# Kernel tuning notes

Measured on AMD Instinct MI355X. Metric: run time of the kernel, lower is better.

Reference implementation:

```python
import jax, jax.numpy as jnp
import numpy as np
from jax import lax

B, QL, N_IN, H = 64, 2048, 256, 64


def setup_inputs() -> dict:
    key = jax.random.key(0)
    ks = jax.random.split(key, 8)
    s = 1.0 / np.sqrt(H)  # PyTorch LSTMCell init scale
    return {
        "h_concat": jax.random.normal(ks[0], (B, QL, N_IN), dtype=jnp.float32),
        "w21": jax.random.normal(ks[1], (N_IN, 1), dtype=jnp.float32),
        "w22": jax.random.normal(ks[2], (H, 1), dtype=jnp.float32),
        "bias2": jax.random.normal(ks[3], (1,), dtype=jnp.float32),
        "W_ih": jax.random.uniform(ks[4], (4 * H, N_IN + 1), dtype=jnp.float32, minval=-s, maxval=s),
        "W_hh": jax.random.uniform(ks[5], (4 * H, H), dtype=jnp.float32, minval=-s, maxval=s),
        "b_ih": jax.random.uniform(ks[6], (4 * H,), dtype=jnp.float32, minval=-s, maxval=s),
        "b_hh": jax.random.uniform(ks[7], (4 * H,), dtype=jnp.float32, minval=-s, maxval=s),
    }


def reference(h_concat, w21, w22, bias2, W_ih, W_hh, b_ih, b_hh):
    Bsz, T, n_in = h_concat.shape
    nh = W_hh.shape[1]

    def step(carry, x):
        h, c = carry  # [B,H] each; x: [B,n_in]
        # sigmoid gate: pz_t = sigmoid(x @ w21 + h @ w22 + bias2) -> [B,1]
        pz = jax.nn.sigmoid(x @ w21 + h @ w22 + bias2)
        hz = jnp.concatenate([x, pz], axis=1)  # [B, n_in+1]
        # LSTMCell (PyTorch gate order: i, f, g, o)
        gates = hz @ W_ih.T + b_ih + h @ W_hh.T + b_hh  # [B,4H]
        i, f, g, o = jnp.split(gates, 4, axis=1)
        c_new = jax.nn.sigmoid(f) * c + jax.nn.sigmoid(i) * jnp.tanh(g)
        h_new = jax.nn.sigmoid(o) * jnp.tanh(c_new)
        return (h_new, c_new), pz[:, 0]

    h0 = jnp.zeros((Bsz, nh), dtype=h_concat.dtype)
    c0 = jnp.zeros((Bsz, nh), dtype=h_concat.dtype)
    xs = jnp.swapaxes(h_concat, 0, 1)  # [T,B,n_in]
    _, Z = lax.scan(step, (h0, c0), xs)  # Z: [T,B]
    return jnp.swapaxes(Z, 0, 1)  # [B,T]
```

## Files before the change

kernel.cpp:

```cpp
#include <hip/hip_runtime.h>

#define TT 2048
#define BB 64

typedef float v2f __attribute__((ext_vector_type(2)));

__device__ __forceinline__ float frcp(float x) { return __builtin_amdgcn_rcpf(x); }
__device__ __forceinline__ float fsig(float x) { return frcp(1.f + __expf(-x)); }
__device__ __forceinline__ float ftan(float x) { return 1.f - 2.f * frcp(1.f + __expf(2.f * x)); }
__device__ __forceinline__ v2f fma2(v2f a, v2f b, v2f c) { return __builtin_elementwise_fma(a, b, c); }

__device__ __forceinline__ void barrier_lgkm() {
  asm volatile("s_waitcnt lgkmcnt(0)\n\ts_barrier" ::: "memory");
}

#define DPPADD(x, ctrl)                                                        \
  (x) += __builtin_bit_cast(float, __builtin_amdgcn_update_dpp(                \
             0, __builtin_bit_cast(int, (x)), (ctrl), 0xf, 0xf, true))

__device__ __forceinline__ float wave_sum64(float x) {
  DPPADD(x, 0x111);
  DPPADD(x, 0x112);
  DPPADD(x, 0x114);
  DPPADD(x, 0x118);
  DPPADD(x, 0x142);
  DPPADD(x, 0x143);
  return __builtin_bit_cast(
      float, __builtin_amdgcn_readlane(__builtin_bit_cast(int, x), 63));
}

__global__ __launch_bounds__(256) void gates_gemm(const float* __restrict__ X,
                                                  const float* __restrict__ W,
                                                  const float* __restrict__ bih,
                                                  const float* __restrict__ bhh,
                                                  float* __restrict__ G,
                                                  int t0, int Tc) {
  __shared__ __align__(16) float As[32][64];
  __shared__ __align__(16) float Bs[32][64];
  const int tid = threadIdx.x;
  const int m0 = blockIdx.x * 64;
  const int n0 = blockIdx.y * 64;
  const int bb = m0 / Tc;
  const int tt0 = m0 - bb * Tc;
  const int tx = tid & 15, ty = tid >> 4;
  const int r  = tid >> 2;
  const int kq = (tid & 3) * 8;
  const float* xrow = X + ((size_t)(bb * TT + t0 + tt0 + r)) * 256 + kq;
  const float* wrow = W + (size_t)(n0 + r) * 257 + kq;
  float acc[4][4] = {};
  for (int k0 = 0; k0 < 256; k0 += 32) {
    float4 a0 = *reinterpret_cast<const float4*>(xrow + k0);
    float4 a1 = *reinterpret_cast<const float4*>(xrow + k0 + 4);
    float bv[8];
#pragma unroll
    for (int u = 0; u < 8; ++u) bv[u] = wrow[k0 + u];
    if (k0 != 0) __syncthreads();
    As[kq+0][r]=a0.x; As[kq+1][r]=a0.y; As[kq+2][r]=a0.z; As[kq+3][r]=a0.w;
    As[kq+4][r]=a1.x; As[kq+5][r]=a1.y; As[kq+6][r]=a1.z; As[kq+7][r]=a1.w;
#pragma unroll
    for (int u = 0; u < 8; ++u) Bs[kq+u][r] = bv[u];
    __syncthreads();
#pragma unroll
    for (int kk = 0; kk < 32; ++kk) {
      float4 av = *reinterpret_cast<const float4*>(&As[kk][ty*4]);
      float4 bw = *reinterpret_cast<const float4*>(&Bs[kk][tx*4]);
      const float aa[4] = {av.x, av.y, av.z, av.w};
      const float bbv[4] = {bw.x, bw.y, bw.z, bw.w};
#pragma unroll
      for (int i = 0; i < 4; ++i)
#pragma unroll
        for (int j = 0; j < 4; ++j) acc[i][j] += aa[i] * bbv[j];
    }
  }
  const int col = n0 + tx * 4;
  float bsum[4];
#pragma unroll
  for (int j = 0; j < 4; ++j) bsum[j] = bih[col + j] + bhh[col + j];
#pragma unroll
  for (int i = 0; i < 4; ++i) {
    float4 o;
    o.x = acc[i][0] + bsum[0];
    o.y = acc[i][1] + bsum[1];
    o.z = acc[i][2] + bsum[2];
    o.w = acc[i][3] + bsum[3];
    *reinterpret_cast<float4*>(&G[(size_t)(m0 + ty*4 + i) * 256 + col]) = o;
  }
}

__global__ __launch_bounds__(256) void pz_kernel(const float* __restrict__ X,
                                                 const float* __restrict__ w21,
                                                 const float* __restrict__ bias2,
                                                 float* __restrict__ P,
                                                 int t0, int Tc) {
  const int r = blockIdx.x * 4 + (threadIdx.x >> 6);
  const int lane = threadIdx.x & 63;
  const int bb = r / Tc;
  const int tt = r - bb * Tc;
  const float4 xv = *reinterpret_cast<const float4*>(
      &X[((size_t)(bb * TT + t0 + tt)) * 256 + lane * 4]);
  const float4 wv = *reinterpret_cast<const float4*>(&w21[lane * 4]);
  float s = xv.x*wv.x + xv.y*wv.y + xv.z*wv.z + xv.w*wv.w;
#pragma unroll
  for (int o = 32; o; o >>= 1) s += __shfl_xor(s, o);
  if (lane == 0) P[r] = s + bias2[0];
}

__global__ __launch_bounds__(128, 1) void lstm_seq3(const float* __restrict__ G,
                                                    const float* __restrict__ P,
                                                    const float* __restrict__ Wih,
                                                    const float* __restrict__ Whh,
                                                    const float* __restrict__ w22,
                                                    float* __restrict__ Z,
                                                    float* __restrict__ hq,
                                                    float* __restrict__ cq,
                                                    int t0, int Tc) {
  const int b = blockIdx.x;
  const int tid = threadIdx.x;
  const int w = tid >> 6;
  const int l = tid & 63;
  const int sub = l >> 5;
  const int u = w * 32 + (l & 31);
  __shared__ __align__(16) float h_s[2][64];

  const int rowA = sub * 64 + u;
  const int rowB = rowA + 128;
  v2f whA[32], whB[32];
#pragma unroll
  for (int j = 0; j < 16; ++j) {
    float4 va = *reinterpret_cast<const float4*>(&Whh[(size_t)rowA * 64 + 4*j]);
    float4 vb = *reinterpret_cast<const float4*>(&Whh[(size_t)rowB * 64 + 4*j]);
    whA[2*j] = v2f{va.x, va.y}; whA[2*j+1] = v2f{va.z, va.w};
    whB[2*j] = v2f{vb.x, vb.y}; whB[2*j+1] = v2f{vb.z, vb.w};
  }
  const float wihLA = Wih[(size_t)rowA * 257 + 256];
  const float wihLB = Wih[(size_t)rowB * 257 + 256];
  const float w22r  = w22[l];
  const float kB = sub ? 1.f : 2.f;
  const float mB = sub ? 1.f : 2.f;
  const float aB = sub ? 0.f : -1.f;

  float h = 0.f, c = 0.f;
  if (t0 != 0) { h = hq[b * 64 + u]; c = cq[b * 64 + u]; }
  if (l >= 32) h_s[0][u] = h;
  barrier_lgkm();

  const float* Gb = G + (size_t)b * Tc * 256;
  const float* Pb = P + (size_t)b * Tc;
  float* Zb = Z + (size_t)b * TT + t0;

  float grA[4], grB[4], pr[4];
#pragma unroll
  for (int q = 0; q < 4; ++q) {
    grA[q] = Gb[(size_t)q * 256 + rowA];
    grB[q] = Gb[(size_t)q * 256 + rowB];
    pr[q]  = Pb[q];
  }

  for (int tt = 0; tt < Tc; tt += 4) {
    float zs[4];
#pragma unroll
    for (int uu = 0; uu < 4; ++uu) {
      const int step = tt + uu;
      const int rb = uu & 1;
      const float gxA = grA[uu], gxB = grB[uu], p0 = pr[uu];
      int pf = step + 4; if (pf > Tc - 1) pf = Tc - 1;
      grA[uu] = Gb[(size_t)pf * 256 + rowA];
      grB[uu] = Gb[(size_t)pf * 256 + rowB];
      pr[uu]  = Pb[pf];

      float rsum = h_s[rb][l] * w22r;
      const float tot = wave_sum64(rsum);
      const float pz = fsig(tot + p0);

      v2f aA0{0.f,0.f}, aA1{0.f,0.f}, aA2{0.f,0.f}, aA3{0.f,0.f};
      v2f aB0{0.f,0.f}, aB1{0.f,0.f}, aB2{0.f,0.f}, aB3{0.f,0.f};
      const float4* hp = reinterpret_cast<const float4*>(h_s[rb]);
#pragma unroll
      for (int q = 0; q < 16; q += 2) {
        const float4 hv0 = hp[q];
        const float4 hv1 = hp[q+1];
        const v2f h01 = v2f{hv0.x, hv0.y}, h23 = v2f{hv0.z, hv0.w};
        const v2f h45 = v2f{hv1.x, hv1.y}, h67 = v2f{hv1.z, hv1.w};
        aA0 = fma2(h01, whA[2*q],   aA0);  aA1 = fma2(h23, whA[2*q+1], aA1);
        aA2 = fma2(h45, whA[2*q+2], aA2);  aA3 = fma2(h67, whA[2*q+3], aA3);
        aB0 = fma2(h01, whB[2*q],   aB0);  aB1 = fma2(h23, whB[2*q+1], aB1);
        aB2 = fma2(h45, whB[2*q+2], aB2);  aB3 = fma2(h67, whB[2*q+3], aB3);
      }
      const v2f sA = (aA0 + aA1) + (aA2 + aA3);
      const v2f sB = (aB0 + aB1) + (aB2 + aB3);
      const float preA = gxA + pz * wihLA + (sA.x + sA.y);
      const float preB = gxB + pz * wihLB + (sB.x + sB.y);
      const float actA = fsig(preA);
      const float actB = mB * fsig(kB * preB) + aB;

      const float prod = actA * actB;
      const float igx = __shfl_xor(prod, 32);
      c = actA * c + igx;
      h = actB * ftan(c);
      if (l >= 32) h_s[rb ^ 1][u] = h;
      zs[uu] = pz;
      barrier_lgkm();
    }
    if (tid == 0) {
      float4 zo; zo.x = zs[0]; zo.y = zs[1]; zo.z = zs[2]; zo.w = zs[3];
      *reinterpret_cast<float4*>(&Zb[tt]) = zo;
    }
  }
  if (l >= 32) { hq[b * 64 + u] = h; cq[b * 64 + u] = c; }
}

__global__ __launch_bounds__(256) void lstm_fallback(const float* __restrict__ X,
    const float* __restrict__ w21, const float* __restrict__ w22,
    const float* __restrict__ bias2, const float* __restrict__ Wih,
    const float* __restrict__ Whh, const float* __restrict__ bih,
    const float* __restrict__ bhh, float* __restrict__ Z) {
  const int b = blockIdx.x;
  const int g = threadIdx.x;
  const int lane = g & 63;
  __shared__ __align__(16) float h_s[64];
  __shared__ float act_s[256];
  __shared__ __align__(16) float x_s[256];
  __shared__ __align__(16) float w21_s[256];
  float wh[64];
#pragma unroll
  for (int j = 0; j < 64; j += 4) {
    float4 v = *reinterpret_cast<const float4*>(&Whh[(size_t)g*64 + j]);
    wh[j]=v.x; wh[j+1]=v.y; wh[j+2]=v.z; wh[j+3]=v.w;
  }
  const float wihL = Wih[(size_t)g*257 + 256];
  const float bias = bih[g] + bhh[g];
  const float b2 = bias2[0];
  const float w22r = w22[lane];
  w21_s[g] = w21[g];
  if (g < 64) h_s[g] = 0.f;
  float c = 0.f;
  __syncthreads();
  const float* Wr = Wih + (size_t)g * 257;
  for (int t = 0; t < TT; ++t) {
    x_s[g] = X[((size_t)b*TT + t)*256 + g];
    __syncthreads();
    float pv = h_s[lane] * w22r;
    {
      const float4 xq = *reinterpret_cast<const float4*>(&x_s[lane*4]);
      const float4 wq = *reinterpret_cast<const float4*>(&w21_s[lane*4]);
      pv += xq.x*wq.x + xq.y*wq.y + xq.z*wq.z + xq.w*wq.w;
    }
#pragma unroll
    for (int o = 32; o; o >>= 1) pv += __shfl_xor(pv, o);
    const float pz = fsig(pv + b2);
    float a0=0.f, a1=0.f, a2=0.f, a3=0.f;
#pragma unroll
    for (int j = 0; j < 64; j += 4) {
      float4 hv = *reinterpret_cast<const float4*>(&h_s[j]);
      a0 += hv.x*wh[j]; a1 += hv.y*wh[j+1]; a2 += hv.z*wh[j+2]; a3 += hv.w*wh[j+3];
    }
    float xd0=0.f, xd1=0.f, xd2=0.f, xd3=0.f;
    for (int k = 0; k < 256; k += 4) {
      const float4 xq = *reinterpret_cast<const float4*>(&x_s[k]);
      xd0 += xq.x*Wr[k]; xd1 += xq.y*Wr[k+1]; xd2 += xq.z*Wr[k+2]; xd3 += xq.w*Wr[k+3];
    }
    const float pre = bias + pz*wihL + ((a0+a1)+(a2+a3)) + ((xd0+xd1)+(xd2+xd3));
    act_s[g] = ((g >> 6) == 2) ? ftan(pre) : fsig(pre);
    if (g == 0) Z[(size_t)b*TT + t] = pz;
    __syncthreads();
    if (g < 64) {
      const float iv = act_s[g], fv = act_s[64+g], gv = act_s[128+g], ov = act_s[192+g];
      c = fv*c + iv*gv;
      h_s[g] = ov * ftan(c);
    }
    __syncthreads();
  }
}

extern "C" void kernel_launch(void* const* d_in, const int* in_sizes, int n_in,
                              void* d_out, int out_size, void* d_ws, size_t ws_size,
                              hipStream_t stream) {
  const float* X     = (const float*)d_in[0];
  const float* w21   = (const float*)d_in[1];
  const float* w22   = (const float*)d_in[2];
  const float* bias2 = (const float*)d_in[3];
  const float* Wih   = (const float*)d_in[4];
  const float* Whh   = (const float*)d_in[5];
  const float* bih   = (const float*)d_in[6];
  const float* bhh   = (const float*)d_in[7];
  float* Z = (float*)d_out;

  int Tc = 0;
  for (int cand = 2048; cand >= 64; cand >>= 1) {
    size_t need = (size_t)cand * (64*256*4 + 64*4) + 2*64*64*4;
    if (ws_size >= need) { Tc = cand; break; }
  }
  if (Tc == 0) {
    lstm_fallback<<<dim3(64), dim3(256), 0, stream>>>(X, w21, w22, bias2, Wih, Whh, bih, bhh, Z);
    return;
  }
  float* Gbuf = (float*)d_ws;
  float* Pbuf = Gbuf + (size_t)64 * Tc * 256;
  float* hq   = Pbuf + (size_t)64 * Tc;
  float* cq   = hq + 64 * 64;
  for (int t0 = 0; t0 < 2048; t0 += Tc) {
    gates_gemm<<<dim3(Tc, 4), dim3(256), 0, stream>>>(X, Wih, bih, bhh, Gbuf, t0, Tc);
    pz_kernel<<<dim3(16 * Tc), dim3(256), 0, stream>>>(X, w21, bias2, Pbuf, t0, Tc);
    lstm_seq3<<<dim3(64), dim3(128), 0, stream>>>(Gbuf, Pbuf, Wih, Whh, w22, Z, hq, cq, t0, Tc);
  }
}
```

Measured before the change: 1.229 ms.

## Fuse pz projection into gates GEMM and pack four batch rows per LSTM block

```diff
diff --git a/kernel.cpp b/kernel.cpp
--- a/kernel.cpp
+++ b/kernel.cpp
@@ -2,6 +2,7 @@
 
 #define TT 2048
 #define BB 64
+#define ROWS 4
 
 typedef float v2f __attribute__((ext_vector_type(2)));
 
@@ -33,10 +34,14 @@
                                                   const float* __restrict__ W,
                                                   const float* __restrict__ bih,
                                                   const float* __restrict__ bhh,
+                                                  const float* __restrict__ w21,
+                                                  const float* __restrict__ bias2,
                                                   float* __restrict__ G,
+                                                  float* __restrict__ P,
                                                   int t0, int Tc) {
   __shared__ __align__(16) float As[32][64];
   __shared__ __align__(16) float Bs[32][64];
+  __shared__ float w21_s[256];
   const int tid = threadIdx.x;
   const int m0 = blockIdx.x * 64;
   const int n0 = blockIdx.y * 64;
@@ -45,9 +50,12 @@
   const int tx = tid & 15, ty = tid >> 4;
   const int r  = tid >> 2;
   const int kq = (tid & 3) * 8;
+  const bool do_pz = (blockIdx.y == 0) && (tid < 64);
+  w21_s[tid] = w21[tid];
   const float* xrow = X + ((size_t)(bb * TT + t0 + tt0 + r)) * 256 + kq;
   const float* wrow = W + (size_t)(n0 + r) * 257 + kq;
   float acc[4][4] = {};
+  float psum = 0.f;
   for (int k0 = 0; k0 < 256; k0 += 32) {
     float4 a0 = *reinterpret_cast<const float4*>(xrow + k0);
     float4 a1 = *reinterpret_cast<const float4*>(xrow + k0 + 4);
@@ -71,7 +79,12 @@
 #pragma unroll
         for (int j = 0; j < 4; ++j) acc[i][j] += aa[i] * bbv[j];
     }
-  }
+    if (do_pz) {
+#pragma unroll
+      for (int kk = 0; kk < 32; ++kk) psum += As[kk][tid] * w21_s[k0 + kk];
+    }
+  }
+  if (do_pz) P[m0 + tid] = psum + bias2[0];
   const int col = n0 + tx * 4;
   float bsum[4];
 #pragma unroll
@@ -87,40 +100,20 @@
   }
 }
 
-__global__ __launch_bounds__(256) void pz_kernel(const float* __restrict__ X,
-                                                 const float* __restrict__ w21,
-                                                 const float* __restrict__ bias2,
-                                                 float* __restrict__ P,
-                                                 int t0, int Tc) {
-  const int r = blockIdx.x * 4 + (threadIdx.x >> 6);
-  const int lane = threadIdx.x & 63;
-  const int bb = r / Tc;
-  const int tt = r - bb * Tc;
-  const float4 xv = *reinterpret_cast<const float4*>(
-      &X[((size_t)(bb * TT + t0 + tt)) * 256 + lane * 4]);
-  const float4 wv = *reinterpret_cast<const float4*>(&w21[lane * 4]);
-  float s = xv.x*wv.x + xv.y*wv.y + xv.z*wv.z + xv.w*wv.w;
-#pragma unroll
-  for (int o = 32; o; o >>= 1) s += __shfl_xor(s, o);
-  if (lane == 0) P[r] = s + bias2[0];
-}
-
-__global__ __launch_bounds__(128, 1) void lstm_seq3(const float* __restrict__ G,
-                                                    const float* __restrict__ P,
-                                                    const float* __restrict__ Wih,
-                                                    const float* __restrict__ Whh,
-                                                    const float* __restrict__ w22,
-                                                    float* __restrict__ Z,
-                                                    float* __restrict__ hq,
-                                                    float* __restrict__ cq,
-                                                    int t0, int Tc) {
-  const int b = blockIdx.x;
+__global__ __launch_bounds__(128 * ROWS, 1) void lstm_seq4(
+    const float* __restrict__ G, const float* __restrict__ P,
+    const float* __restrict__ Wih, const float* __restrict__ Whh,
+    const float* __restrict__ w22, float* __restrict__ Z,
+    float* __restrict__ hq, float* __restrict__ cq, int t0, int Tc) {
   const int tid = threadIdx.x;
-  const int w = tid >> 6;
-  const int l = tid & 63;
+  const int r   = tid >> 7;
+  const int rt  = tid & 127;
+  const int b   = blockIdx.x * ROWS + r;
+  const int w   = rt >> 6;
+  const int l   = rt & 63;
   const int sub = l >> 5;
-  const int u = w * 32 + (l & 31);
-  __shared__ __align__(16) float h_s[2][64];
+  const int u   = w * 32 + (l & 31);
+  __shared__ __align__(16) float h_s[ROWS][2][64];
 
   const int rowA = sub * 64 + u;
   const int rowB = rowA + 128;
@@ -141,7 +134,7 @@
 
   float h = 0.f, c = 0.f;
   if (t0 != 0) { h = hq[b * 64 + u]; c = cq[b * 64 + u]; }
-  if (l >= 32) h_s[0][u] = h;
+  if (l >= 32) h_s[r][0][u] = h;
   barrier_lgkm();
 
   const float* Gb = G + (size_t)b * Tc * 256;
@@ -168,13 +161,13 @@
       grB[uu] = Gb[(size_t)pf * 256 + rowB];
       pr[uu]  = Pb[pf];
 
-      float rsum = h_s[rb][l] * w22r;
+      float rsum = h_s[r][rb][l] * w22r;
       const float tot = wave_sum64(rsum);
       const float pz = fsig(tot + p0);
 
       v2f aA0{0.f,0.f}, aA1{0.f,0.f}, aA2{0.f,0.f}, aA3{0.f,0.f};
       v2f aB0{0.f,0.f}, aB1{0.f,0.f}, aB2{0.f,0.f}, aB3{0.f,0.f};
-      const float4* hp = reinterpret_cast<const float4*>(h_s[rb]);
+      const float4* hp = reinterpret_cast<const float4*>(h_s[r][rb]);
 #pragma unroll
       for (int q = 0; q < 16; q += 2) {
         const float4 hv0 = hp[q];
@@ -197,11 +190,11 @@
       const float igx = __shfl_xor(prod, 32);
       c = actA * c + igx;
       h = actB * ftan(c);
-      if (l >= 32) h_s[rb ^ 1][u] = h;
+      if (l >= 32) h_s[r][rb ^ 1][u] = h;
       zs[uu] = pz;
       barrier_lgkm();
     }
-    if (tid == 0) {
+    if (rt == 0) {
       float4 zo; zo.x = zs[0]; zo.y = zs[1]; zo.z = zs[2]; zo.w = zs[3];
       *reinterpret_cast<float4*>(&Zb[tt]) = zo;
     }
@@ -299,8 +292,9 @@
   float* hq   = Pbuf + (size_t)64 * Tc;
   float* cq   = hq + 64 * 64;
   for (int t0 = 0; t0 < 2048; t0 += Tc) {
-    gates_gemm<<<dim3(Tc, 4), dim3(256), 0, stream>>>(X, Wih, bih, bhh, Gbuf, t0, Tc);
-    pz_kernel<<<dim3(16 * Tc), dim3(256), 0, stream>>>(X, w21, bias2, Pbuf, t0, Tc);
-    lstm_seq3<<<dim3(64), dim3(128), 0, stream>>>(Gbuf, Pbuf, Wih, Whh, w22, Z, hq, cq, t0, Tc);
-  }
-}
+    gates_gemm<<<dim3(Tc, 4), dim3(256), 0, stream>>>(X, Wih, bih, bhh, w21, bias2,
+                                                      Gbuf, Pbuf, t0, Tc);
+    lstm_seq4<<<dim3(BB / ROWS), dim3(128 * ROWS), 0, stream>>>(
+        Gbuf, Pbuf, Wih, Whh, w22, Z, hq, cq, t0, Tc);
+  }
+}
```

Measured after the change: 1.819 ms. +48.0%, slower.

## Run one wave per batch row with fp16 dot2 recurrent matvec

Applied to the files above, without the earlier changes.

```diff
diff --git a/kernel.cpp b/kernel.cpp
--- a/kernel.cpp
+++ b/kernel.cpp
@@ -3,16 +3,17 @@
 #define TT 2048
 #define BB 64
 
-typedef float v2f __attribute__((ext_vector_type(2)));
+typedef _Float16 v2h __attribute__((ext_vector_type(2)));
 
 __device__ __forceinline__ float frcp(float x) { return __builtin_amdgcn_rcpf(x); }
 __device__ __forceinline__ float fsig(float x) { return frcp(1.f + __expf(-x)); }
 __device__ __forceinline__ float ftan(float x) { return 1.f - 2.f * frcp(1.f + __expf(2.f * x)); }
-__device__ __forceinline__ v2f fma2(v2f a, v2f b, v2f c) { return __builtin_elementwise_fma(a, b, c); }
-
-__device__ __forceinline__ void barrier_lgkm() {
-  asm volatile("s_waitcnt lgkmcnt(0)\n\ts_barrier" ::: "memory");
-}
+
+#if __has_builtin(__builtin_amdgcn_fdot2)
+#define FDOT2(a, b, c) __builtin_amdgcn_fdot2((a), (b), (c), false)
+#else
+#define FDOT2(a, b, c) ((c) + (float)(a).x * (float)(b).x + (float)(a).y * (float)(b).y)
+#endif
 
 #define DPPADD(x, ctrl)                                                        \
   (x) += __builtin_bit_cast(float, __builtin_amdgcn_update_dpp(                \
@@ -105,55 +106,50 @@
   if (lane == 0) P[r] = s + bias2[0];
 }
 
-__global__ __launch_bounds__(128, 1) void lstm_seq3(const float* __restrict__ G,
-                                                    const float* __restrict__ P,
-                                                    const float* __restrict__ Wih,
-                                                    const float* __restrict__ Whh,
-                                                    const float* __restrict__ w22,
-                                                    float* __restrict__ Z,
-                                                    float* __restrict__ hq,
-                                                    float* __restrict__ cq,
-                                                    int t0, int Tc) {
-  const int b = blockIdx.x;
+__global__ __launch_bounds__(512, 2) void lstm_seq5(
+    const float* __restrict__ G, const float* __restrict__ P,
+    const float* __restrict__ Wih, const float* __restrict__ Whh,
+    const float* __restrict__ w22, float* __restrict__ Z,
+    float* __restrict__ hq, float* __restrict__ cq, int t0, int Tc) {
   const int tid = threadIdx.x;
-  const int w = tid >> 6;
-  const int l = tid & 63;
-  const int sub = l >> 5;
-  const int u = w * 32 + (l & 31);
-  __shared__ __align__(16) float h_s[2][64];
-
-  const int rowA = sub * 64 + u;
-  const int rowB = rowA + 128;
-  v2f whA[32], whB[32];
-#pragma unroll
-  for (int j = 0; j < 16; ++j) {
-    float4 va = *reinterpret_cast<const float4*>(&Whh[(size_t)rowA * 64 + 4*j]);
-    float4 vb = *reinterpret_cast<const float4*>(&Whh[(size_t)rowB * 64 + 4*j]);
-    whA[2*j] = v2f{va.x, va.y}; whA[2*j+1] = v2f{va.z, va.w};
-    whB[2*j] = v2f{vb.x, vb.y}; whB[2*j+1] = v2f{vb.z, vb.w};
-  }
-  const float wihLA = Wih[(size_t)rowA * 257 + 256];
-  const float wihLB = Wih[(size_t)rowB * 257 + 256];
-  const float w22r  = w22[l];
-  const float kB = sub ? 1.f : 2.f;
-  const float mB = sub ? 1.f : 2.f;
-  const float aB = sub ? 0.f : -1.f;
+  const int wv  = tid >> 6;
+  const int l   = tid & 63;
+  const int b   = blockIdx.x * 8 + wv;
+  __shared__ __align__(16) _Float16 hsm[8][64];
+
+  v2h wh[4][32];
+#pragma unroll
+  for (int q = 0; q < 4; ++q) {
+#pragma unroll
+    for (int j = 0; j < 16; ++j) {
+      float4 v = *reinterpret_cast<const float4*>(&Whh[(size_t)(q*64 + l)*64 + 4*j]);
+      v2h pA, pB;
+      pA.x = (_Float16)v.x; pA.y = (_Float16)v.y;
+      pB.x = (_Float16)v.z; pB.y = (_Float16)v.w;
+      wh[q][2*j] = pA; wh[q][2*j+1] = pB;
+    }
+  }
+  float wihL[4];
+#pragma unroll
+  for (int q = 0; q < 4; ++q) wihL[q] = Wih[(size_t)(q*64 + l)*257 + 256];
+  const float w22r = w22[l];
 
   float h = 0.f, c = 0.f;
-  if (t0 != 0) { h = hq[b * 64 + u]; c = cq[b * 64 + u]; }
-  if (l >= 32) h_s[0][u] = h;
-  barrier_lgkm();
-
-  const float* Gb = G + (size_t)b * Tc * 256;
+  if (t0 != 0) { h = hq[b * 64 + l]; c = cq[b * 64 + l]; }
+  hsm[wv][l] = (_Float16)h;
+  asm volatile("s_waitcnt lgkmcnt(0)" ::: "memory");
+  __builtin_amdgcn_wave_barrier();
+
+  const float* Gb = G + (size_t)b * Tc * 256 + l;
   const float* Pb = P + (size_t)b * Tc;
   float* Zb = Z + (size_t)b * TT + t0;
 
-  float grA[4], grB[4], pr[4];
-#pragma unroll
-  for (int q = 0; q < 4; ++q) {
-    grA[q] = Gb[(size_t)q * 256 + rowA];
-    grB[q] = Gb[(size_t)q * 256 + rowB];
-    pr[q]  = Pb[q];
+  float gr[4][4], pr[4];
+#pragma unroll
+  for (int u = 0; u < 4; ++u) {
+#pragma unroll
+    for (int q = 0; q < 4; ++q) gr[u][q] = Gb[(size_t)u * 256 + q * 64];
+    pr[u] = Pb[u];
   }
 
   for (int tt = 0; tt < Tc; tt += 4) {
@@ -161,52 +157,60 @@
 #pragma unroll
     for (int uu = 0; uu < 4; ++uu) {
       const int step = tt + uu;
-      const int rb = uu & 1;
-      const float gxA = grA[uu], gxB = grB[uu], p0 = pr[uu];
+      const float gx0 = gr[uu][0], gx1 = gr[uu][1];
+      const float gx2 = gr[uu][2], gx3 = gr[uu][3];
+      const float p0 = pr[uu];
       int pf = step + 4; if (pf > Tc - 1) pf = Tc - 1;
-      grA[uu] = Gb[(size_t)pf * 256 + rowA];
-      grB[uu] = Gb[(size_t)pf * 256 + rowB];
-      pr[uu]  = Pb[pf];
-
-      float rsum = h_s[rb][l] * w22r;
-      const float tot = wave_sum64(rsum);
+#pragma unroll
+      for (int q = 0; q < 4; ++q) gr[uu][q] = Gb[(size_t)pf * 256 + q * 64];
+      pr[uu] = Pb[pf];
+
+      const float tot = wave_sum64(h * w22r);
       const float pz = fsig(tot + p0);
 
-      v2f aA0{0.f,0.f}, aA1{0.f,0.f}, aA2{0.f,0.f}, aA3{0.f,0.f};
-      v2f aB0{0.f,0.f}, aB1{0.f,0.f}, aB2{0.f,0.f}, aB3{0.f,0.f};
-      const float4* hp = reinterpret_cast<const float4*>(h_s[rb]);
-#pragma unroll
-      for (int q = 0; q < 16; q += 2) {
-        const float4 hv0 = hp[q];
-        const float4 hv1 = hp[q+1];
-        const v2f h01 = v2f{hv0.x, hv0.y}, h23 = v2f{hv0.z, hv0.w};
-        const v2f h45 = v2f{hv1.x, hv1.y}, h67 = v2f{hv1.z, hv1.w};
-        aA0 = fma2(h01, whA[2*q],   aA0);  aA1 = fma2(h23, whA[2*q+1], aA1);
-        aA2 = fma2(h45, whA[2*q+2], aA2);  aA3 = fma2(h67, whA[2*q+3], aA3);
-        aB0 = fma2(h01, whB[2*q],   aB0);  aB1 = fma2(h23, whB[2*q+1], aB1);
-        aB2 = fma2(h45, whB[2*q+2], aB2);  aB3 = fma2(h67, whB[2*q+3], aB3);
+      float d0a=0.f,d0b=0.f,d1a=0.f,d1b=0.f,d2a=0.f,d2b=0.f,d3a=0.f,d3b=0.f;
+      const uint4* hp = reinterpret_cast<const uint4*>(hsm[wv]);
+#pragma unroll
+      for (int jj = 0; jj < 8; ++jj) {
+        const uint4 uq = hp[jj];
+        const v2h ha = __builtin_bit_cast(v2h, uq.x);
+        const v2h hb = __builtin_bit_cast(v2h, uq.y);
+        const v2h hc = __builtin_bit_cast(v2h, uq.z);
+        const v2h hd = __builtin_bit_cast(v2h, uq.w);
+        d0a = FDOT2(ha, wh[0][4*jj+0], d0a); d0b = FDOT2(hb, wh[0][4*jj+1], d0b);
+        d0a = FDOT2(hc, wh[0][4*jj+2], d0a); d0b = FDOT2(hd, wh[0][4*jj+3], d0b);
+        d1a = FDOT2(ha, wh[1][4*jj+0], d1a); d1b = FDOT2(hb, wh[1][4*jj+1], d1b);
+        d1a = FDOT2(hc, wh[1][4*jj+2], d1a); d1b = FDOT2(hd, wh[1][4*jj+3], d1b);
+        d2a = FDOT2(ha, wh[2][4*jj+0], d2a); d2b = FDOT2(hb, wh[2][4*jj+1], d2b);
+        d2a = FDOT2(hc, wh[2][4*jj+2], d2a); d2b = FDOT2(hd, wh[2][4*jj+3], d2b);
+        d3a = FDOT2(ha, wh[3][4*jj+0], d3a); d3b = FDOT2(hb, wh[3][4*jj+1], d3b);
+        d3a = FDOT2(hc, wh[3][4*jj+2], d3a); d3b = FDOT2(hd, wh[3][4*jj+3], d3b);
       }
-      const v2f sA = (aA0 + aA1) + (aA2 + aA3);
-      const v2f sB = (aB0 + aB1) + (aB2 + aB3);
-      const float preA = gxA + pz * wihLA + (sA.x + sA.y);
-      const float preB = gxB + pz * wihLB + (sB.x + sB.y);
-      const float actA = fsig(preA);
-      const float actB = mB * fsig(kB * preB) + aB;
-
-      const float prod = actA * actB;
-      const float igx = __shfl_xor(prod, 32);
-      c = actA * c + igx;
-      h = actB * ftan(c);
-      if (l >= 32) h_s[rb ^ 1][u] = h;
+      const float pre0 = gx0 + pz * wihL[0] + (d0a + d0b);
+      const float pre1 = gx1 + pz * wihL[1] + (d1a + d1b);
+      const float pre2 = gx2 + pz * wihL[2] + (d2a + d2b);
+      const float pre3 = gx3 + pz * wihL[3] + (d3a + d3b);
+
+      const float ai = fsig(pre0);
+      const float af = fsig(pre1);
+      const float ag = ftan(pre2);
+      const float ao = fsig(pre3);
+      c = af * c + ai * ag;
+      h = ao * ftan(c);
+
+      __builtin_amdgcn_wave_barrier();
+      hsm[wv][l] = (_Float16)h;
+      asm volatile("s_waitcnt lgkmcnt(0)" ::: "memory");
+      __builtin_amdgcn_wave_barrier();
       zs[uu] = pz;
-      barrier_lgkm();
-    }
-    if (tid == 0) {
+    }
+    if (l == 0) {
       float4 zo; zo.x = zs[0]; zo.y = zs[1]; zo.z = zs[2]; zo.w = zs[3];
       *reinterpret_cast<float4*>(&Zb[tt]) = zo;
     }
   }
-  if (l >= 32) { hq[b * 64 + u] = h; cq[b * 64 + u] = c; }
+  hq[b * 64 + l] = h;
+  cq[b * 64 + l] = c;
 }
 
 __global__ __launch_bounds__(256) void lstm_fallback(const float* __restrict__ X,
@@ -301,6 +305,7 @@
   for (int t0 = 0; t0 < 2048; t0 += Tc) {
     gates_gemm<<<dim3(Tc, 4), dim3(256), 0, stream>>>(X, Wih, bih, bhh, Gbuf, t0, Tc);
     pz_kernel<<<dim3(16 * Tc), dim3(256), 0, stream>>>(X, w21, bias2, Pbuf, t0, Tc);
-    lstm_seq3<<<dim3(64), dim3(128), 0, stream>>>(Gbuf, Pbuf, Wih, Whh, w22, Z, hq, cq, t0, Tc);
-  }
-}
+    lstm_seq5<<<dim3(BB / 8), dim3(512), 0, stream>>>(
+        Gbuf, Pbuf, Wih, Whh, w22, Z, hq, cq, t0, Tc);
+  }
+}
```

Measured after the change: 1.938 ms. +57.7%, slower.
